# Kernel optimization log

Measured on AMD Instinct MI355X. Metric: run time of the kernel, lower is better.

Reference implementation:

```python
import jax, jax.numpy as jnp
import numpy as np

N_NODES = 50000
N_EDGES = 800000
D = 64        # input_nf == output_nf
HID = 64      # hidden_nf
NQ = 3        # n_qubits
NORM = 100.0  # normalization_factor, aggregation_method='sum'
MU = 0.5      # hardcoded self.mu

silu = jax.nn.silu
_Zv = jnp.array([1.0, -1.0])


def _zax(q):
    # Z eigenvalues broadcast along qubit axis q of a [N,2,2,2] statevector
    return _Zv.reshape(tuple(2 if k == q else 1 for k in range(NQ)))


def _quantum_circuit(x, alpha, beta, gamma, delta, Lam):
    """Batched 3-qubit statevector simulation of the PennyLane circuit.
    x: [N, NQ] per-node rotation inputs. Returns [N, NQ] Pauli-Z expvals."""
    N = x.shape[0]
    st = jnp.zeros((N, 2, 2, 2), jnp.complex64).at[:, 0, 0, 0].set(1.0)

    def ap(st, U, q):  # apply 2x2 gate U ([2,2] const or [N,2,2] batched) on qubit q
        st = jnp.moveaxis(st, 1 + q, 3)
        sub = 'nij,nabj->nabi' if U.ndim == 3 else 'ij,nabj->nabi'
        st = jnp.einsum(sub, U, st)
        return jnp.moveaxis(st, 3, 1 + q)

    def rz(st, theta, q):  # diagonal RZ(theta) with per-node theta [N]
        ph = jnp.exp(-0.5j * theta.astype(jnp.complex64)[:, None] * _Zv)  # [N,2]
        return st * ph.reshape((N,) + tuple(2 if k == q else 1 for k in range(NQ)))

    def ry_mat(theta):  # [N] -> [N,2,2]
        c, s = jnp.cos(theta / 2), jnp.sin(theta / 2)
        return jnp.stack([jnp.stack([c, -s], -1), jnp.stack([s, c], -1)], -2).astype(jnp.complex64)

    cb, sb = jnp.cos(beta / 2), jnp.sin(beta / 2)
    RX = jnp.stack([jnp.stack([cb + 0j, -1j * sb]), jnp.stack([-1j * sb, cb + 0j])])
    Hm = jnp.array([[1.0, 1.0], [1.0, -1.0]], jnp.complex64) / np.sqrt(2.0)

    # 1) data-encoding RY layer
    for q in range(NQ):
        st = ap(st, ry_mat(x[:, q] * alpha), q)
    # 2) coupling Hamiltonian: IsingZZ(gamma*(Lam_ij+Lam_ji)/2) on each pair (diagonal phase)
    for i in range(NQ):
        for j in range(i + 1, NQ):
            phi = gamma * (Lam[i, j] + Lam[j, i]) / 2
            st = st * jnp.exp(-0.5j * phi * (_zax(i) * _zax(j)))[None]
    # 3) kinetic RX layer
    for q in range(NQ):
        st = ap(st, RX, q)
    # 4) anharmonic layer: RZ, H, RZ, H per qubit
    for q in range(NQ):
        st = rz(st, delta * (1.0 - MU * x[:, q] ** 2), q)
        st = ap(st, Hm, q)
        st = rz(st, delta * x[:, q] ** 2, q)
        st = ap(st, Hm, q)
    # 5) final kinetic RX layer
    for q in range(NQ):
        st = ap(st, RX, q)

    probs = jnp.abs(st) ** 2  # [N,2,2,2]
    return jnp.stack([jnp.sum(probs * _zax(q)[None], axis=(1, 2, 3)) for q in range(NQ)], axis=1)


def setup_inputs() -> dict:
    key = jax.random.key(0)
    ks = jax.random.split(key, 10)
    def w(k, shape):
        return jax.random.normal(k, shape, jnp.float32) * 0.05
    h = jax.random.normal(ks[0], (N_NODES, D), jnp.float32)
    edge_index = jax.random.randint(ks[1], (2, N_EDGES), 0, N_NODES)
    Lam = jnp.full((NQ, NQ), -0.1 / (NQ - 1), jnp.float32).at[jnp.arange(NQ), jnp.arange(NQ)].set(0.1)
    return {
        'h': h, 'edge_index': edge_index,
        'eW1': w(ks[2], (2 * D, HID)), 'eb1': jnp.zeros(HID, jnp.float32),
        'eW2': w(ks[3], (HID, HID)), 'eb2': jnp.zeros(HID, jnp.float32),
        'qW1': w(ks[4], (D + HID, HID)), 'qb1': jnp.zeros(HID, jnp.float32),
        'qW2': w(ks[5], (HID, NQ)), 'qb2': jnp.zeros(NQ, jnp.float32),
        'pW1': w(ks[6], (D + HID + NQ, HID)), 'pb1': jnp.zeros(HID, jnp.float32),
        'pW2': w(ks[7], (HID, D)), 'pb2': jnp.zeros(D, jnp.float32),
        'alpha': jnp.float32(0.1 / NQ), 'beta': jnp.float32(np.pi / (4 * NQ)),
        'gamma': jnp.float32(0.1 / NQ), 'delta': jnp.float32(0.05),
        'Lambda': Lam,
    }


def reference(h, edge_index, eW1, eb1, eW2, eb2, qW1, qb1, qW2, qb2,
              pW1, pb1, pW2, pb2, alpha, beta, gamma, delta, Lambda):
    row, col = edge_index[0], edge_index[1]
    # edge model (no attention, no edge_attr, no edge_mask)
    e_in = jnp.concatenate([h[row], h[col]], axis=1)           # [E, 2D]
    mij = silu(silu(e_in @ eW1 + eb1) @ eW2 + eb2)             # [E, HID]
    # node model: scatter-sum aggregation normalized by factor ('sum' mode)
    agg = jax.ops.segment_sum(mij, row, num_segments=N_NODES) / NORM
    a = jnp.concatenate([h, agg], axis=1)                      # [N, D+HID]
    q_in = silu(a @ qW1 + qb1) @ qW2 + qb2                     # [N, NQ]
    # original detaches inputs and rebuilds outputs via torch.tensor -> no grad flow
    q_out = jax.lax.stop_gradient(
        _quantum_circuit(jax.lax.stop_gradient(q_in), alpha, beta, gamma, delta, Lambda)
    ).astype(h.dtype)
    a2 = jnp.concatenate([a, q_out], axis=1)                   # [N, 2*HID+NQ]
    out = h + (silu(a2 @ pW1 + pb1) @ pW2 + pb2)
    return out, mij
```

## Files before the change

### kernel.cpp

```cpp
#include <hip/hip_runtime.h>
#include <hip/hip_bf16.h>
#include <math.h>
#include <stdint.h>


#define N_NODES 50000
#define N_EDGES 800000
#define DIM 64
#define HID 64
#define T_EDGE (N_EDGES / 16)
#define T_NODE (N_NODES / 16)
#define EDGE_GRID 512
#define EWAVES 16
#define NODE_GRID 512

typedef __bf16 bf16_t;
typedef __bf16 bf16x8 __attribute__((ext_vector_type(8)));
typedef float f32x4 __attribute__((ext_vector_type(4)));

__device__ __forceinline__ float silu_f(float x) {
    return x * __builtin_amdgcn_rcpf(1.f + __expf(-x));
}

__device__ __forceinline__ f32x4 mfma16(bf16x8 a, bf16x8 b, f32x4 c) {
    return __builtin_amdgcn_mfma_f32_16x16x32_bf16(a, b, c, 0, 0, 0);
}

__device__ __forceinline__ bf16x8 cvt8(const float* __restrict__ p) {
    f32x4 u0 = *(const f32x4*)p;
    f32x4 u1 = *(const f32x4*)(p + 4);
    bf16x8 r;
    r[0] = (bf16_t)u0[0]; r[1] = (bf16_t)u0[1]; r[2] = (bf16_t)u0[2]; r[3] = (bf16_t)u0[3];
    r[4] = (bf16_t)u1[0]; r[5] = (bf16_t)u1[1]; r[6] = (bf16_t)u1[2]; r[7] = (bf16_t)u1[3];
    return r;
}

__global__ __launch_bounds__(256) void init_kernel(const float* __restrict__ h,
                                                   bf16_t* __restrict__ hb,
                                                   bf16_t* __restrict__ aggz, int n8)
{
    int i = blockIdx.x * 256 + threadIdx.x;
    if (i < n8) {
        *(bf16x8*)(hb + (size_t)i * 8) = cvt8(h + (size_t)i * 8);
        bf16x8 zz;
        #pragma unroll
        for (int j = 0; j < 8; ++j) zz[j] = (bf16_t)0.f;
        *(bf16x8*)(aggz + (size_t)i * 8) = zz;
    }
}

__global__ __launch_bounds__(1024) void edge_kernel(
    const bf16_t* __restrict__ hb,
    const int* __restrict__ ei,
    const float* __restrict__ eW1, const float* __restrict__ eb1,
    const float* __restrict__ eW2, const float* __restrict__ eb2,
    float* __restrict__ mij_out,
    bf16_t* __restrict__ agg)
{
    __shared__ __align__(16) bf16_t sB1[64][136];
    __shared__ __align__(16) bf16_t sB2[64][72];
    __shared__ __align__(16) bf16_t sHid[EWAVES][16][72];
    __shared__ float sb1[64], sb2[64];

    const int tid = threadIdx.x;
    for (int idx = tid; idx < 128 * 64; idx += 1024) {
        int k = idx >> 6, n = idx & 63;
        sB1[n][k] = (bf16_t)eW1[idx];
    }
    for (int idx = tid; idx < 64 * 64; idx += 1024) {
        int k = idx >> 6, n = idx & 63;
        sB2[n][k] = (bf16_t)eW2[idx];
    }
    if (tid < 64) { sb1[tid] = eb1[tid]; sb2[tid] = eb2[tid]; }
    __syncthreads();

    const int l = tid & 63, wave = tid >> 6;
    const int m = l & 15, quad = l >> 4;
    const int eisel = m + ((quad & 1) ? N_EDGES : 0);
    const f32x4 z = {0.f, 0.f, 0.f, 0.f};

    int t = blockIdx.x * EWAVES + wave;
    if (t >= T_EDGE) return;

    int ev = ei[t * 16 + eisel];
    int nrow = __shfl(ev, m);
    int ncol = __shfl(ev, 16 + m);
    bf16x8 a_cur[4];
    {
        const bf16_t* ra = hb + (size_t)nrow * DIM;
        const bf16_t* rb = hb + (size_t)ncol * DIM;
        #pragma unroll
        for (int ks = 0; ks < 4; ++ks) {
            const int k0 = ks * 32 + quad * 8;
            a_cur[ks] = *(const bf16x8*)((k0 < 64) ? (ra + k0) : (rb + (k0 - 64)));
        }
    }

    while (true) {
        const int e0 = t * 16;
        const int tn = t + EDGE_GRID * EWAVES;
        const bool has_next = (tn < T_EDGE);

        int evn = 0;
        if (has_next) evn = ei[tn * 16 + eisel];

        f32x4 acc[4] = {z, z, z, z};
        #pragma unroll
        for (int ks = 0; ks < 4; ++ks) {
            const int k0 = ks * 32 + quad * 8;
            #pragma unroll
            for (int nt = 0; nt < 4; ++nt)
                acc[nt] = mfma16(a_cur[ks], *(const bf16x8*)&sB1[nt * 16 + m][k0], acc[nt]);
        }
        #pragma unroll
        for (int nt = 0; nt < 4; ++nt)
            #pragma unroll
            for (int rr = 0; rr < 4; ++rr) {
                int row = quad * 4 + rr, col = nt * 16 + m;
                sHid[wave][row][col] = (bf16_t)silu_f(acc[nt][rr] + sb1[col]);
            }

        int nrow_n = 0, ncol_n = 0;
        bf16x8 a_nxt[4];
        if (has_next) {
            nrow_n = __shfl(evn, m);
            ncol_n = __shfl(evn, 16 + m);
            const bf16_t* ra = hb + (size_t)nrow_n * DIM;
            const bf16_t* rb = hb + (size_t)ncol_n * DIM;
            #pragma unroll
            for (int ks = 0; ks < 4; ++ks) {
                const int k0 = ks * 32 + quad * 8;
                a_nxt[ks] = *(const bf16x8*)((k0 < 64) ? (ra + k0) : (rb + (k0 - 64)));
            }
        }

        f32x4 acc2[4] = {z, z, z, z};
        #pragma unroll
        for (int ks = 0; ks < 2; ++ks) {
            const int k0 = ks * 32 + quad * 8;
            bf16x8 a = *(const bf16x8*)&sHid[wave][m][k0];
            #pragma unroll
            for (int nt = 0; nt < 4; ++nt)
                acc2[nt] = mfma16(a, *(const bf16x8*)&sB2[nt * 16 + m][k0], acc2[nt]);
        }

        int dstrow[4];
        #pragma unroll
        for (int rr = 0; rr < 4; ++rr) dstrow[rr] = __shfl(nrow, quad * 4 + rr);

        #pragma unroll
        for (int rr = 0; rr < 4; ++rr) {
            uint32_t pku[4];
            #pragma unroll
            for (int nt = 0; nt < 4; ++nt) {
                const int col = nt * 16 + m;
                float v = silu_f(acc2[nt][rr] + sb2[col]);
                __builtin_nontemporal_store(
                    v, &mij_out[(size_t)(e0 + quad * 4 + rr) * HID + col]);
                float vh = __shfl_xor(v, 1);
                union { bf16_t h2[2]; uint32_t u; } pk;
                pk.h2[0] = (bf16_t)v; pk.h2[1] = (bf16_t)vh;
                pku[nt] = pk.u;
            }
            bf16_t* rowp = agg + (size_t)dstrow[rr] * HID;
            const int src = (l & 48) | ((2 * m) & 15);
            #pragma unroll
            for (int B = 0; B < 2; ++B) {
                uint32_t ua = (uint32_t)__shfl((int)pku[2 * B], src);
                uint32_t ub = (uint32_t)__shfl((int)pku[2 * B + 1], src);
                uint32_t u = (m >= 8) ? ub : ua;
                const int c = 32 * B + 2 * m;
                asm volatile("global_atomic_pk_add_bf16 %0, %1, off"
                             :: "v"((uint64_t)(uintptr_t)(rowp + c)), "v"(u)
                             : "memory");
            }
        }

        if (!has_next) break;
        t = tn;
        nrow = nrow_n; ncol = ncol_n;
        #pragma unroll
        for (int ks = 0; ks < 4; ++ks) a_cur[ks] = a_nxt[ks];
    }
}

__global__ __launch_bounds__(512) void node_kernel(
    const float* __restrict__ h, const bf16_t* __restrict__ aggb,
    const float* __restrict__ qW1, const float* __restrict__ qb1,
    const float* __restrict__ qW2, const float* __restrict__ qb2,
    const float* __restrict__ pW1, const float* __restrict__ pb1,
    const float* __restrict__ pW2, const float* __restrict__ pb2,
    const float* __restrict__ al_p, const float* __restrict__ be_p,
    const float* __restrict__ ga_p, const float* __restrict__ de_p,
    const float* __restrict__ lam_p,
    float* __restrict__ out)
{
    __shared__ __align__(16) bf16_t sQ1[64][136];
    __shared__ __align__(16) bf16_t sP1[64][136];
    __shared__ __align__(16) bf16_t sP2[64][72];
    __shared__ __align__(16) bf16_t sQ2b[16][72];
    __shared__ __align__(16) bf16_t sHid[8][16][72];
    __shared__ float sQio[8][16][4];
    __shared__ __align__(16) float sqb1[64];
    __shared__ __align__(16) float spb1[64];
    __shared__ __align__(16) float spb2[64];
    __shared__ float sqb2[4];

    const int tid = threadIdx.x;
    for (int idx = tid; idx < 128 * 64; idx += 512) {
        int k = idx >> 6, n = idx & 63;
        float w = qW1[idx];
        sQ1[n][k] = (bf16_t)(k < 64 ? w : w * 0.01f);
    }
    for (int idx = tid; idx < 131 * 64; idx += 512) {
        int k = idx >> 6, n = idx & 63;
        float w = pW1[idx];
        sP1[n][k] = (bf16_t)((k >= 64 && k < 128) ? w * 0.01f : w);
    }
    for (int idx = tid; idx < 5 * 64; idx += 512) {
        int k = 131 + (idx >> 6), n = idx & 63;
        sP1[n][k] = (bf16_t)0.f;
    }
    for (int idx = tid; idx < 64 * 64; idx += 512) {
        int k = idx >> 6, n = idx & 63;
        sP2[n][k] = (bf16_t)pW2[idx];
    }
    for (int idx = tid; idx < 16 * 72; idx += 512) {
        int c = idx / 72, k = idx - c * 72;
        sQ2b[c][k] = (bf16_t)((c < 3 && k < 64) ? qW2[k * 3 + c] : 0.f);
    }
    if (tid < 64) { sqb1[tid] = qb1[tid]; spb1[tid] = pb1[tid]; spb2[tid] = pb2[tid]; }
    if (tid < 3) sqb2[tid] = qb2[tid];
    __syncthreads();

    const int lane = tid & 63, wave = tid >> 6;
    const int m = lane & 15, quad = lane >> 4;
    const float al = al_p[0], be = be_p[0];
    const float ga = ga_p[0], de = de_p[0];
    const float phi01 = ga * (lam_p[1] + lam_p[3]) * 0.5f;
    const float phi02 = ga * (lam_p[2] + lam_p[6]) * 0.5f;
    const float phi12 = ga * (lam_p[5] + lam_p[7]) * 0.5f;
    const float cbg = __cosf(0.5f * be), sbg = __sinf(0.5f * be);
    const f32x4 z = {0.f, 0.f, 0.f, 0.f};

    for (int t = blockIdx.x * 8 + wave; t < T_NODE; t += NODE_GRID * 8) {
        const int n0 = t * 16;
        const float* hrow = h + (size_t)(n0 + m) * DIM;
        const bf16_t* grow = aggb + (size_t)(n0 + m) * HID;

        {
            f32x4 acc[4] = {z, z, z, z};
            #pragma unroll
            for (int ks = 0; ks < 4; ++ks) {
                const int k0 = ks * 32 + quad * 8;
                bf16x8 a = (k0 < 64) ? cvt8(hrow + k0)
                                     : *(const bf16x8*)(grow + (k0 - 64));
                #pragma unroll
                for (int nt = 0; nt < 4; ++nt)
                    acc[nt] = mfma16(a, *(const bf16x8*)&sQ1[nt * 16 + m][k0], acc[nt]);
            }
            #pragma unroll
            for (int nt = 0; nt < 4; ++nt)
                #pragma unroll
                for (int rr = 0; rr < 4; ++rr) {
                    int row = quad * 4 + rr, col = nt * 16 + m;
                    sHid[wave][row][col] = (bf16_t)silu_f(acc[nt][rr] + sqb1[col]);
                }
        }

        {
            f32x4 aq = z;
            #pragma unroll
            for (int ks = 0; ks < 2; ++ks) {
                const int k0 = ks * 32 + quad * 8;
                bf16x8 a = *(const bf16x8*)&sHid[wave][m][k0];
                bf16x8 b = *(const bf16x8*)&sQ2b[m][k0];
                aq = mfma16(a, b, aq);
            }
            if (m < 3) {
                #pragma unroll
                for (int rr = 0; rr < 4; ++rr)
                    sQio[wave][quad * 4 + rr][m] = aq[rr] + sqb2[m];
            }
        }

        if (lane < 16) {
            float qin[3];
            qin[0] = sQio[wave][lane][0];
            qin[1] = sQio[wave][lane][1];
            qin[2] = sQio[wave][lane][2];
            float re[8], im[8];
            float cc[3], ssn[3];
            #pragma unroll
            for (int q = 0; q < 3; ++q) {
                float th = 0.5f * qin[q] * al;
                cc[q] = __cosf(th); ssn[q] = __sinf(th);
            }
            #pragma unroll
            for (int i = 0; i < 8; ++i) {
                float v0 = (i & 4) ? ssn[0] : cc[0];
                float v1 = (i & 2) ? ssn[1] : cc[1];
                float v2 = (i & 1) ? ssn[2] : cc[2];
                re[i] = v0 * v1 * v2; im[i] = 0.f;
            }
            #pragma unroll
            for (int i = 0; i < 8; ++i) {
                float z0 = (i & 4) ? -1.f : 1.f;
                float z1 = (i & 2) ? -1.f : 1.f;
                float z2 = (i & 1) ? -1.f : 1.f;
                float th = -0.5f * (phi01 * z0 * z1 + phi02 * z0 * z2 + phi12 * z1 * z2);
                float ct = __cosf(th), st = __sinf(th);
                float r = re[i], iM = im[i];
                re[i] = r * ct - iM * st;
                im[i] = r * st + iM * ct;
            }
            auto rx = [&]() {
                #pragma unroll
                for (int q = 0; q < 3; ++q) {
                    int msk = 4 >> q;
                    #pragma unroll
                    for (int i = 0; i < 8; ++i) {
                        if (i & msk) continue;
                        int j = i | msk;
                        float r0 = re[i], i0 = im[i], r1 = re[j], i1 = im[j];
                        re[i] = cbg * r0 + sbg * i1;
                        im[i] = cbg * i0 - sbg * r1;
                        re[j] = sbg * i0 + cbg * r1;
                        im[j] = -sbg * r0 + cbg * i1;
                    }
                }
            };
            auto hgate = [&](int q) {
                const float inv = 0.70710678f;
                int msk = 4 >> q;
                #pragma unroll
                for (int i = 0; i < 8; ++i) {
                    if (i & msk) continue;
                    int j = i | msk;
                    float r0 = re[i], i0 = im[i], r1 = re[j], i1 = im[j];
                    re[i] = (r0 + r1) * inv; im[i] = (i0 + i1) * inv;
                    re[j] = (r0 - r1) * inv; im[j] = (i0 - i1) * inv;
                }
            };
            auto rzg = [&](int q, float th) {
                int msk = 4 >> q;
                float c = __cosf(0.5f * th), s = __sinf(0.5f * th);
                #pragma unroll
                for (int i = 0; i < 8; ++i) {
                    float sg = (i & msk) ? s : -s;
                    float r = re[i], iM = im[i];
                    re[i] = r * c - iM * sg;
                    im[i] = r * sg + iM * c;
                }
            };
            rx();
            #pragma unroll
            for (int q = 0; q < 3; ++q) {
                float x = qin[q];
                rzg(q, de * (1.f - 0.5f * x * x));
                hgate(q);
                rzg(q, de * x * x);
                hgate(q);
            }
            rx();
            float e0v = 0.f, e1v = 0.f, e2v = 0.f;
            #pragma unroll
            for (int i = 0; i < 8; ++i) {
                float p = re[i] * re[i] + im[i] * im[i];
                e0v += (i & 4) ? -p : p;
                e1v += (i & 2) ? -p : p;
                e2v += (i & 1) ? -p : p;
            }
            sQio[wave][lane][0] = e0v;
            sQio[wave][lane][1] = e1v;
            sQio[wave][lane][2] = e2v;
        }

        __builtin_amdgcn_sched_barrier(0);

        f32x4 acc2[4] = {z, z, z, z};
        #pragma unroll
        for (int ks = 0; ks < 4; ++ks) {
            const int k0 = ks * 32 + quad * 8;
            bf16x8 a = (k0 < 64) ? cvt8(hrow + k0)
                                 : *(const bf16x8*)(grow + (k0 - 64));
            #pragma unroll
            for (int nt = 0; nt < 4; ++nt)
                acc2[nt] = mfma16(a, *(const bf16x8*)&sP1[nt * 16 + m][k0], acc2[nt]);
        }
        {
            bf16x8 a, bz;
            #pragma unroll
            for (int j = 0; j < 8; ++j) { a[j] = (bf16_t)0.f; bz[j] = (bf16_t)0.f; }
            if (quad == 0) {
                a[0] = (bf16_t)sQio[wave][m][0];
                a[1] = (bf16_t)sQio[wave][m][1];
                a[2] = (bf16_t)sQio[wave][m][2];
            }
            #pragma unroll
            for (int nt = 0; nt < 4; ++nt) {
                bf16x8 b = bz;
                if (quad == 0) b = *(const bf16x8*)&sP1[nt * 16 + m][128];
                acc2[nt] = mfma16(a, b, acc2[nt]);
            }
        }
        #pragma unroll
        for (int nt = 0; nt < 4; ++nt)
            #pragma unroll
            for (int rr = 0; rr < 4; ++rr) {
                int row = quad * 4 + rr, col = nt * 16 + m;
                sHid[wave][row][col] = (bf16_t)silu_f(acc2[nt][rr] + spb1[col]);
            }

        f32x4 acc3[4] = {z, z, z, z};
        #pragma unroll
        for (int ks = 0; ks < 2; ++ks) {
            const int k0 = ks * 32 + quad * 8;
            bf16x8 hfrag = *(const bf16x8*)&sHid[wave][m][k0];
            #pragma unroll
            for (int nt = 0; nt < 4; ++nt)
                acc3[nt] = mfma16(*(const bf16x8*)&sP2[nt * 16 + m][k0], hfrag, acc3[nt]);
        }
        {
            const int node = n0 + m;
            const float* hr = h + (size_t)node * DIM;
            float* orow = out + (size_t)node * DIM;
            #pragma unroll
            for (int nt = 0; nt < 4; ++nt) {
                const int c0 = nt * 16 + quad * 4;
                f32x4 hv = *(const f32x4*)(hr + c0);
                f32x4 bias = *(const f32x4*)&spb2[c0];
                f32x4 v;
                #pragma unroll
                for (int rr = 0; rr < 4; ++rr) v[rr] = acc3[nt][rr] + bias[rr] + hv[rr];
                __builtin_nontemporal_store(v, (f32x4*)(orow + c0));
            }
        }
    }
}

extern "C" void kernel_launch(void* const* d_in, const int* in_sizes, int n_in,
                              void* d_out, int out_size, void* d_ws, size_t ws_size,
                              hipStream_t stream)
{
    const float* h   = (const float*)d_in[0];
    const int* ei    = (const int*)d_in[1];
    const float* eW1 = (const float*)d_in[2];
    const float* eb1 = (const float*)d_in[3];
    const float* eW2 = (const float*)d_in[4];
    const float* eb2 = (const float*)d_in[5];
    const float* qW1 = (const float*)d_in[6];
    const float* qb1 = (const float*)d_in[7];
    const float* qW2 = (const float*)d_in[8];
    const float* qb2 = (const float*)d_in[9];
    const float* pW1 = (const float*)d_in[10];
    const float* pb1 = (const float*)d_in[11];
    const float* pW2 = (const float*)d_in[12];
    const float* pb2 = (const float*)d_in[13];
    const float* al  = (const float*)d_in[14];
    const float* be  = (const float*)d_in[15];
    const float* ga  = (const float*)d_in[16];
    const float* de  = (const float*)d_in[17];
    const float* lam = (const float*)d_in[18];

    float* out = (float*)d_out;
    float* mij = out + (size_t)N_NODES * DIM;
    bf16_t* aggb = (bf16_t*)d_ws;
    bf16_t* hb   = aggb + (size_t)N_NODES * HID;

    const int n8 = (N_NODES * DIM) / 8;

    init_kernel<<<(n8 + 255) / 256, 256, 0, stream>>>(h, hb, aggb, n8);
    edge_kernel<<<EDGE_GRID, 1024, 0, stream>>>(hb, ei, eW1, eb1, eW2, eb2, mij, aggb);
    node_kernel<<<NODE_GRID, 512, 0, stream>>>(h, aggb, qW1, qb1, qW2, qb2,
                                               pW1, pb1, pW2, pb2,
                                               al, be, ga, de, lam, out);
}
```

Before: 368.5 us.

## Split node kernel into separate quantum and projection kernels

The fused node kernel is split in two. The first computes the q-MLP and the quantum circuit and writes per-node expectation values to a workspace buffer; the second computes the projection MLP and the residual output. Each kernel now uses less shared memory and fewer registers and handles exactly one 16-node tile per wave, with the grid set to 392 blocks so all tiles are covered without a grid-stride loop. The cost is an extra launch, re-reading h and agg in both kernels, and a small global round trip for the quantum outputs.

```diff
diff --git a/kernel.cpp b/kernel.cpp
--- a/kernel.cpp
+++ b/kernel.cpp
@@ -12,7 +12,7 @@
 #define T_NODE (N_NODES / 16)
 #define EDGE_GRID 512
 #define EWAVES 16
-#define NODE_GRID 512
+#define NODE_GRID 392
 
 typedef __bf16 bf16_t;
 typedef __bf16 bf16x8 __attribute__((ext_vector_type(8)));
@@ -184,27 +184,20 @@
     }
 }
 
-__global__ __launch_bounds__(512) void node_kernel(
+__global__ __launch_bounds__(512) void node_q_kernel(
     const float* __restrict__ h, const bf16_t* __restrict__ aggb,
     const float* __restrict__ qW1, const float* __restrict__ qb1,
     const float* __restrict__ qW2, const float* __restrict__ qb2,
-    const float* __restrict__ pW1, const float* __restrict__ pb1,
-    const float* __restrict__ pW2, const float* __restrict__ pb2,
     const float* __restrict__ al_p, const float* __restrict__ be_p,
     const float* __restrict__ ga_p, const float* __restrict__ de_p,
     const float* __restrict__ lam_p,
-    float* __restrict__ out)
+    float* __restrict__ qsc)
 {
     __shared__ __align__(16) bf16_t sQ1[64][136];
-    __shared__ __align__(16) bf16_t sP1[64][136];
-    __shared__ __align__(16) bf16_t sP2[64][72];
     __shared__ __align__(16) bf16_t sQ2b[16][72];
     __shared__ __align__(16) bf16_t sHid[8][16][72];
     __shared__ float sQio[8][16][4];
-    __shared__ __align__(16) float sqb1[64];
-    __shared__ __align__(16) float spb1[64];
-    __shared__ __align__(16) float spb2[64];
-    __shared__ float sqb2[4];
+    __shared__ float sqb1[64], sqb2[4];
 
     const int tid = threadIdx.x;
     for (int idx = tid; idx < 128 * 64; idx += 512) {
@@ -212,229 +205,254 @@
         float w = qW1[idx];
         sQ1[n][k] = (bf16_t)(k < 64 ? w : w * 0.01f);
     }
-    for (int idx = tid; idx < 131 * 64; idx += 512) {
-        int k = idx >> 6, n = idx & 63;
-        float w = pW1[idx];
-        sP1[n][k] = (bf16_t)((k >= 64 && k < 128) ? w * 0.01f : w);
-    }
-    for (int idx = tid; idx < 5 * 64; idx += 512) {
-        int k = 131 + (idx >> 6), n = idx & 63;
-        sP1[n][k] = (bf16_t)0.f;
-    }
-    for (int idx = tid; idx < 64 * 64; idx += 512) {
-        int k = idx >> 6, n = idx & 63;
-        sP2[n][k] = (bf16_t)pW2[idx];
-    }
     for (int idx = tid; idx < 16 * 72; idx += 512) {
         int c = idx / 72, k = idx - c * 72;
         sQ2b[c][k] = (bf16_t)((c < 3 && k < 64) ? qW2[k * 3 + c] : 0.f);
     }
-    if (tid < 64) { sqb1[tid] = qb1[tid]; spb1[tid] = pb1[tid]; spb2[tid] = pb2[tid]; }
+    if (tid < 64) sqb1[tid] = qb1[tid];
     if (tid < 3) sqb2[tid] = qb2[tid];
     __syncthreads();
 
     const int lane = tid & 63, wave = tid >> 6;
     const int m = lane & 15, quad = lane >> 4;
-    const float al = al_p[0], be = be_p[0];
-    const float ga = ga_p[0], de = de_p[0];
-    const float phi01 = ga * (lam_p[1] + lam_p[3]) * 0.5f;
-    const float phi02 = ga * (lam_p[2] + lam_p[6]) * 0.5f;
-    const float phi12 = ga * (lam_p[5] + lam_p[7]) * 0.5f;
-    const float cbg = __cosf(0.5f * be), sbg = __sinf(0.5f * be);
+    const int t = blockIdx.x * 8 + wave;
+    if (t >= T_NODE) return;
+    const int n0 = t * 16;
+    const float* hrow = h + (size_t)(n0 + m) * DIM;
+    const bf16_t* grow = aggb + (size_t)(n0 + m) * HID;
     const f32x4 z = {0.f, 0.f, 0.f, 0.f};
 
-    for (int t = blockIdx.x * 8 + wave; t < T_NODE; t += NODE_GRID * 8) {
-        const int n0 = t * 16;
-        const float* hrow = h + (size_t)(n0 + m) * DIM;
-        const bf16_t* grow = aggb + (size_t)(n0 + m) * HID;
-
-        {
-            f32x4 acc[4] = {z, z, z, z};
-            #pragma unroll
-            for (int ks = 0; ks < 4; ++ks) {
-                const int k0 = ks * 32 + quad * 8;
-                bf16x8 a = (k0 < 64) ? cvt8(hrow + k0)
-                                     : *(const bf16x8*)(grow + (k0 - 64));
-                #pragma unroll
-                for (int nt = 0; nt < 4; ++nt)
-                    acc[nt] = mfma16(a, *(const bf16x8*)&sQ1[nt * 16 + m][k0], acc[nt]);
-            }
+    {
+        f32x4 acc[4] = {z, z, z, z};
+        #pragma unroll
+        for (int ks = 0; ks < 4; ++ks) {
+            const int k0 = ks * 32 + quad * 8;
+            bf16x8 a = (k0 < 64) ? cvt8(hrow + k0)
+                                 : *(const bf16x8*)(grow + (k0 - 64));
             #pragma unroll
             for (int nt = 0; nt < 4; ++nt)
-                #pragma unroll
-                for (int rr = 0; rr < 4; ++rr) {
-                    int row = quad * 4 + rr, col = nt * 16 + m;
-                    sHid[wave][row][col] = (bf16_t)silu_f(acc[nt][rr] + sqb1[col]);
-                }
-        }
-
-        {
-            f32x4 aq = z;
-            #pragma unroll
-            for (int ks = 0; ks < 2; ++ks) {
-                const int k0 = ks * 32 + quad * 8;
-                bf16x8 a = *(const bf16x8*)&sHid[wave][m][k0];
-                bf16x8 b = *(const bf16x8*)&sQ2b[m][k0];
-                aq = mfma16(a, b, aq);
-            }
-            if (m < 3) {
-                #pragma unroll
-                for (int rr = 0; rr < 4; ++rr)
-                    sQio[wave][quad * 4 + rr][m] = aq[rr] + sqb2[m];
-            }
-        }
-
-        if (lane < 16) {
-            float qin[3];
-            qin[0] = sQio[wave][lane][0];
-            qin[1] = sQio[wave][lane][1];
-            qin[2] = sQio[wave][lane][2];
-            float re[8], im[8];
-            float cc[3], ssn[3];
+                acc[nt] = mfma16(a, *(const bf16x8*)&sQ1[nt * 16 + m][k0], acc[nt]);
+        }
+        #pragma unroll
+        for (int nt = 0; nt < 4; ++nt)
+            #pragma unroll
+            for (int rr = 0; rr < 4; ++rr) {
+                int row = quad * 4 + rr, col = nt * 16 + m;
+                sHid[wave][row][col] = (bf16_t)silu_f(acc[nt][rr] + sqb1[col]);
+            }
+    }
+
+    {
+        f32x4 aq = z;
+        #pragma unroll
+        for (int ks = 0; ks < 2; ++ks) {
+            const int k0 = ks * 32 + quad * 8;
+            bf16x8 a = *(const bf16x8*)&sHid[wave][m][k0];
+            bf16x8 b = *(const bf16x8*)&sQ2b[m][k0];
+            aq = mfma16(a, b, aq);
+        }
+        if (m < 3) {
+            #pragma unroll
+            for (int rr = 0; rr < 4; ++rr)
+                sQio[wave][quad * 4 + rr][m] = aq[rr] + sqb2[m];
+        }
+    }
+
+    if (lane < 16) {
+        const float al = al_p[0], be = be_p[0];
+        const float ga = ga_p[0], de = de_p[0];
+        const float phi01 = ga * (lam_p[1] + lam_p[3]) * 0.5f;
+        const float phi02 = ga * (lam_p[2] + lam_p[6]) * 0.5f;
+        const float phi12 = ga * (lam_p[5] + lam_p[7]) * 0.5f;
+        const float cbg = __cosf(0.5f * be), sbg = __sinf(0.5f * be);
+
+        float qin[3];
+        qin[0] = sQio[wave][lane][0];
+        qin[1] = sQio[wave][lane][1];
+        qin[2] = sQio[wave][lane][2];
+        float re[8], im[8];
+        float cc[3], ssn[3];
+        #pragma unroll
+        for (int q = 0; q < 3; ++q) {
+            float th = 0.5f * qin[q] * al;
+            cc[q] = __cosf(th); ssn[q] = __sinf(th);
+        }
+        #pragma unroll
+        for (int i = 0; i < 8; ++i) {
+            float v0 = (i & 4) ? ssn[0] : cc[0];
+            float v1 = (i & 2) ? ssn[1] : cc[1];
+            float v2 = (i & 1) ? ssn[2] : cc[2];
+            re[i] = v0 * v1 * v2; im[i] = 0.f;
+        }
+        #pragma unroll
+        for (int i = 0; i < 8; ++i) {
+            float z0 = (i & 4) ? -1.f : 1.f;
+            float z1 = (i & 2) ? -1.f : 1.f;
+            float z2 = (i & 1) ? -1.f : 1.f;
+            float th = -0.5f * (phi01 * z0 * z1 + phi02 * z0 * z2 + phi12 * z1 * z2);
+            float ct = __cosf(th), st = __sinf(th);
+            float r = re[i], iM = im[i];
+            re[i] = r * ct - iM * st;
+            im[i] = r * st + iM * ct;
+        }
+        auto rx = [&]() {
             #pragma unroll
             for (int q = 0; q < 3; ++q) {
-                float th = 0.5f * qin[q] * al;
-                cc[q] = __cosf(th); ssn[q] = __sinf(th);
-            }
-            #pragma unroll
-            for (int i = 0; i < 8; ++i) {
-                float v0 = (i & 4) ? ssn[0] : cc[0];
-                float v1 = (i & 2) ? ssn[1] : cc[1];
-                float v2 = (i & 1) ? ssn[2] : cc[2];
-                re[i] = v0 * v1 * v2; im[i] = 0.f;
-            }
-            #pragma unroll
-            for (int i = 0; i < 8; ++i) {
-                float z0 = (i & 4) ? -1.f : 1.f;
-                float z1 = (i & 2) ? -1.f : 1.f;
-                float z2 = (i & 1) ? -1.f : 1.f;
-                float th = -0.5f * (phi01 * z0 * z1 + phi02 * z0 * z2 + phi12 * z1 * z2);
-                float ct = __cosf(th), st = __sinf(th);
-                float r = re[i], iM = im[i];
-                re[i] = r * ct - iM * st;
-                im[i] = r * st + iM * ct;
-            }
-            auto rx = [&]() {
-                #pragma unroll
-                for (int q = 0; q < 3; ++q) {
-                    int msk = 4 >> q;
-                    #pragma unroll
-                    for (int i = 0; i < 8; ++i) {
-                        if (i & msk) continue;
-                        int j = i | msk;
-                        float r0 = re[i], i0 = im[i], r1 = re[j], i1 = im[j];
-                        re[i] = cbg * r0 + sbg * i1;
-                        im[i] = cbg * i0 - sbg * r1;
-                        re[j] = sbg * i0 + cbg * r1;
-                        im[j] = -sbg * r0 + cbg * i1;
-                    }
-                }
-            };
-            auto hgate = [&](int q) {
-                const float inv = 0.70710678f;
                 int msk = 4 >> q;
                 #pragma unroll
                 for (int i = 0; i < 8; ++i) {
                     if (i & msk) continue;
                     int j = i | msk;
                     float r0 = re[i], i0 = im[i], r1 = re[j], i1 = im[j];
-                    re[i] = (r0 + r1) * inv; im[i] = (i0 + i1) * inv;
-                    re[j] = (r0 - r1) * inv; im[j] = (i0 - i1) * inv;
+                    re[i] = cbg * r0 + sbg * i1;
+                    im[i] = cbg * i0 - sbg * r1;
+                    re[j] = sbg * i0 + cbg * r1;
+                    im[j] = -sbg * r0 + cbg * i1;
                 }
-            };
-            auto rzg = [&](int q, float th) {
-                int msk = 4 >> q;
-                float c = __cosf(0.5f * th), s = __sinf(0.5f * th);
-                #pragma unroll
-                for (int i = 0; i < 8; ++i) {
-                    float sg = (i & msk) ? s : -s;
-                    float r = re[i], iM = im[i];
-                    re[i] = r * c - iM * sg;
-                    im[i] = r * sg + iM * c;
-                }
-            };
-            rx();
-            #pragma unroll
-            for (int q = 0; q < 3; ++q) {
-                float x = qin[q];
-                rzg(q, de * (1.f - 0.5f * x * x));
-                hgate(q);
-                rzg(q, de * x * x);
-                hgate(q);
-            }
-            rx();
-            float e0v = 0.f, e1v = 0.f, e2v = 0.f;
+            }
+        };
+        auto hgate = [&](int q) {
+            const float inv = 0.70710678f;
+            int msk = 4 >> q;
             #pragma unroll
             for (int i = 0; i < 8; ++i) {
-                float p = re[i] * re[i] + im[i] * im[i];
-                e0v += (i & 4) ? -p : p;
-                e1v += (i & 2) ? -p : p;
-                e2v += (i & 1) ? -p : p;
-            }
-            sQio[wave][lane][0] = e0v;
-            sQio[wave][lane][1] = e1v;
-            sQio[wave][lane][2] = e2v;
-        }
-
-        __builtin_amdgcn_sched_barrier(0);
-
-        f32x4 acc2[4] = {z, z, z, z};
-        #pragma unroll
-        for (int ks = 0; ks < 4; ++ks) {
-            const int k0 = ks * 32 + quad * 8;
-            bf16x8 a = (k0 < 64) ? cvt8(hrow + k0)
-                                 : *(const bf16x8*)(grow + (k0 - 64));
-            #pragma unroll
-            for (int nt = 0; nt < 4; ++nt)
-                acc2[nt] = mfma16(a, *(const bf16x8*)&sP1[nt * 16 + m][k0], acc2[nt]);
-        }
-        {
-            bf16x8 a, bz;
-            #pragma unroll
-            for (int j = 0; j < 8; ++j) { a[j] = (bf16_t)0.f; bz[j] = (bf16_t)0.f; }
-            if (quad == 0) {
-                a[0] = (bf16_t)sQio[wave][m][0];
-                a[1] = (bf16_t)sQio[wave][m][1];
-                a[2] = (bf16_t)sQio[wave][m][2];
-            }
-            #pragma unroll
-            for (int nt = 0; nt < 4; ++nt) {
-                bf16x8 b = bz;
-                if (quad == 0) b = *(const bf16x8*)&sP1[nt * 16 + m][128];
-                acc2[nt] = mfma16(a, b, acc2[nt]);
-            }
-        }
+                if (i & msk) continue;
+                int j = i | msk;
+                float r0 = re[i], i0 = im[i], r1 = re[j], i1 = im[j];
+                re[i] = (r0 + r1) * inv; im[i] = (i0 + i1) * inv;
+                re[j] = (r0 - r1) * inv; im[j] = (i0 - i1) * inv;
+            }
+        };
+        auto rzg = [&](int q, float th) {
+            int msk = 4 >> q;
+            float c = __cosf(0.5f * th), s = __sinf(0.5f * th);
+            #pragma unroll
+            for (int i = 0; i < 8; ++i) {
+                float sg = (i & msk) ? s : -s;
+                float r = re[i], iM = im[i];
+                re[i] = r * c - iM * sg;
+                im[i] = r * sg + iM * c;
+            }
+        };
+        rx();
+        #pragma unroll
+        for (int q = 0; q < 3; ++q) {
+            float x = qin[q];
+            rzg(q, de * (1.f - 0.5f * x * x));
+            hgate(q);
+            rzg(q, de * x * x);
+            hgate(q);
+        }
+        rx();
+        float e0v = 0.f, e1v = 0.f, e2v = 0.f;
+        #pragma unroll
+        for (int i = 0; i < 8; ++i) {
+            float p = re[i] * re[i] + im[i] * im[i];
+            e0v += (i & 4) ? -p : p;
+            e1v += (i & 2) ? -p : p;
+            e2v += (i & 1) ? -p : p;
+        }
+        f32x4 qo = {e0v, e1v, e2v, 0.f};
+        *(f32x4*)(qsc + (size_t)(n0 + lane) * 4) = qo;
+    }
+}
+
+__global__ __launch_bounds__(512) void node_p_kernel(
+    const float* __restrict__ h, const bf16_t* __restrict__ aggb,
+    const float* __restrict__ qsc,
+    const float* __restrict__ pW1, const float* __restrict__ pb1,
+    const float* __restrict__ pW2, const float* __restrict__ pb2,
+    float* __restrict__ out)
+{
+    __shared__ __align__(16) bf16_t sP1[64][136];
+    __shared__ __align__(16) bf16_t sP2[64][72];
+    __shared__ __align__(16) bf16_t sHid[8][16][72];
+    __shared__ __align__(16) float spb1[64];
+    __shared__ __align__(16) float spb2[64];
+
+    const int tid = threadIdx.x;
+    for (int idx = tid; idx < 131 * 64; idx += 512) {
+        int k = idx >> 6, n = idx & 63;
+        float w = pW1[idx];
+        sP1[n][k] = (bf16_t)((k >= 64 && k < 128) ? w * 0.01f : w);
+    }
+    for (int idx = tid; idx < 5 * 64; idx += 512) {
+        int k = 131 + (idx >> 6), n = idx & 63;
+        sP1[n][k] = (bf16_t)0.f;
+    }
+    for (int idx = tid; idx < 64 * 64; idx += 512) {
+        int k = idx >> 6, n = idx & 63;
+        sP2[n][k] = (bf16_t)pW2[idx];
+    }
+    if (tid < 64) { spb1[tid] = pb1[tid]; spb2[tid] = pb2[tid]; }
+    __syncthreads();
+
+    const int lane = tid & 63, wave = tid >> 6;
+    const int m = lane & 15, quad = lane >> 4;
+    const int t = blockIdx.x * 8 + wave;
+    if (t >= T_NODE) return;
+    const int n0 = t * 16;
+    const float* hrow = h + (size_t)(n0 + m) * DIM;
+    const bf16_t* grow = aggb + (size_t)(n0 + m) * HID;
+    const f32x4 z = {0.f, 0.f, 0.f, 0.f};
+
+    f32x4 acc2[4] = {z, z, z, z};
+    #pragma unroll
+    for (int ks = 0; ks < 4; ++ks) {
+        const int k0 = ks * 32 + quad * 8;
+        bf16x8 a = (k0 < 64) ? cvt8(hrow + k0)
+                             : *(const bf16x8*)(grow + (k0 - 64));
         #pragma unroll
         for (int nt = 0; nt < 4; ++nt)
-            #pragma unroll
-            for (int rr = 0; rr < 4; ++rr) {
-                int row = quad * 4 + rr, col = nt * 16 + m;
-                sHid[wave][row][col] = (bf16_t)silu_f(acc2[nt][rr] + spb1[col]);
-            }
-
-        f32x4 acc3[4] = {z, z, z, z};
-        #pragma unroll
-        for (int ks = 0; ks < 2; ++ks) {
-            const int k0 = ks * 32 + quad * 8;
-            bf16x8 hfrag = *(const bf16x8*)&sHid[wave][m][k0];
-            #pragma unroll
-            for (int nt = 0; nt < 4; ++nt)
-                acc3[nt] = mfma16(*(const bf16x8*)&sP2[nt * 16 + m][k0], hfrag, acc3[nt]);
-        }
-        {
-            const int node = n0 + m;
-            const float* hr = h + (size_t)node * DIM;
-            float* orow = out + (size_t)node * DIM;
-            #pragma unroll
-            for (int nt = 0; nt < 4; ++nt) {
-                const int c0 = nt * 16 + quad * 4;
-                f32x4 hv = *(const f32x4*)(hr + c0);
-                f32x4 bias = *(const f32x4*)&spb2[c0];
-                f32x4 v;
-                #pragma unroll
-                for (int rr = 0; rr < 4; ++rr) v[rr] = acc3[nt][rr] + bias[rr] + hv[rr];
-                __builtin_nontemporal_store(v, (f32x4*)(orow + c0));
-            }
+            acc2[nt] = mfma16(a, *(const bf16x8*)&sP1[nt * 16 + m][k0], acc2[nt]);
+    }
+    {
+        bf16x8 a, bz;
+        #pragma unroll
+        for (int j = 0; j < 8; ++j) { a[j] = (bf16_t)0.f; bz[j] = (bf16_t)0.f; }
+        if (quad == 0) {
+            f32x4 qo = *(const f32x4*)(qsc + (size_t)(n0 + m) * 4);
+            a[0] = (bf16_t)qo[0];
+            a[1] = (bf16_t)qo[1];
+            a[2] = (bf16_t)qo[2];
+        }
+        #pragma unroll
+        for (int nt = 0; nt < 4; ++nt) {
+            bf16x8 b = bz;
+            if (quad == 0) b = *(const bf16x8*)&sP1[nt * 16 + m][128];
+            acc2[nt] = mfma16(a, b, acc2[nt]);
+        }
+    }
+    #pragma unroll
+    for (int nt = 0; nt < 4; ++nt)
+        #pragma unroll
+        for (int rr = 0; rr < 4; ++rr) {
+            int row = quad * 4 + rr, col = nt * 16 + m;
+            sHid[wave][row][col] = (bf16_t)silu_f(acc2[nt][rr] + spb1[col]);
+        }
+
+    f32x4 acc3[4] = {z, z, z, z};
+    #pragma unroll
+    for (int ks = 0; ks < 2; ++ks) {
+        const int k0 = ks * 32 + quad * 8;
+        bf16x8 hfrag = *(const bf16x8*)&sHid[wave][m][k0];
+        #pragma unroll
+        for (int nt = 0; nt < 4; ++nt)
+            acc3[nt] = mfma16(*(const bf16x8*)&sP2[nt * 16 + m][k0], hfrag, acc3[nt]);
+    }
+    {
+        const int node = n0 + m;
+        const float* hr = h + (size_t)node * DIM;
+        float* orow = out + (size_t)node * DIM;
+        #pragma unroll
+        for (int nt = 0; nt < 4; ++nt) {
+            const int c0 = nt * 16 + quad * 4;
+            f32x4 hv = *(const f32x4*)(hr + c0);
+            f32x4 bias = *(const f32x4*)&spb2[c0];
+            f32x4 v;
+            #pragma unroll
+            for (int rr = 0; rr < 4; ++rr) v[rr] = acc3[nt][rr] + bias[rr] + hv[rr];
+            __builtin_nontemporal_store(v, (f32x4*)(orow + c0));
         }
     }
 }
@@ -467,12 +485,13 @@
     float* mij = out + (size_t)N_NODES * DIM;
     bf16_t* aggb = (bf16_t*)d_ws;
     bf16_t* hb   = aggb + (size_t)N_NODES * HID;
+    float* qsc   = (float*)(hb + (size_t)N_NODES * DIM);
 
     const int n8 = (N_NODES * DIM) / 8;
 
     init_kernel<<<(n8 + 255) / 256, 256, 0, stream>>>(h, hb, aggb, n8);
     edge_kernel<<<EDGE_GRID, 1024, 0, stream>>>(hb, ei, eW1, eb1, eW2, eb2, mij, aggb);
-    node_kernel<<<NODE_GRID, 512, 0, stream>>>(h, aggb, qW1, qb1, qW2, qb2,
-                                               pW1, pb1, pW2, pb2,
-                                               al, be, ga, de, lam, out);
-}
+    node_q_kernel<<<NODE_GRID, 512, 0, stream>>>(h, aggb, qW1, qb1, qW2, qb2,
+                                                 al, be, ga, de, lam, qsc);
+    node_p_kernel<<<NODE_GRID, 512, 0, stream>>>(h, aggb, qsc, pW1, pb1, pW2, pb2, out);
+}
```

Result: no change. 373.6 us (+1.4%).
